# Optimization experiments

Measured on AMD Instinct MI355X. Metric: run time of the kernel, lower is better.

The kernel has to match this reference:

```python
import jax, jax.numpy as jnp
import numpy as np

B = 1048576
S = 8
K = 10  # n_facts
EPS = 1e-8
ENTROPY_W = 0.01
DIVERSITY_W = 0.1


def setup_inputs() -> dict:
    key = jax.random.key(0)
    k1, k2, k3, k4, k5 = jax.random.split(key, 5)
    p = jax.random.uniform(k1, (B, 2, K), dtype=jnp.float32) + 1e-3
    pCS = p / jnp.sum(p, axis=-1, keepdims=True)  # normalized probs like Categorical
    base_loss = jax.random.uniform(k2, (1,), dtype=jnp.float32)
    Y = jax.random.randint(k3, (B,), 0, 19, dtype=jnp.int32)
    samples1 = jax.random.randint(k4, (S, B), 0, K, dtype=jnp.int32)
    samples2 = jax.random.randint(k5, (S, B), 0, K, dtype=jnp.int32)
    return {"pCS": pCS, "base_loss": base_loss, "Y": Y,
            "samples1": samples1, "samples2": samples2}


def reference(pCS, base_loss, Y, samples1, samples2):
    n_facts = pCS.shape[-1]
    s = samples1.shape[0]
    p1 = pCS[:, 0, :]  # [B, K]
    p2 = pCS[:, 1, :]
    # entropy regularization
    ent1 = -jnp.sum(p1 * jnp.log(p1 + EPS), axis=-1).mean()
    ent2 = -jnp.sum(p2 * jnp.log(p2 + EPS), axis=-1).mean()
    entropy_loss = -(ent1 + ent2) / 2
    # diversity: count unique (d1,d2) pairs per batch element (vectorized bincount-style)
    pairs = (samples1 * n_facts + samples2).T  # [B, S]
    eq = pairs[:, :, None] == pairs[:, None, :]  # [B, S, S]
    earlier = jnp.tril(jnp.ones((s, s), dtype=bool), k=-1)  # j < i
    dup = jnp.any(eq & earlier[None], axis=-1)  # [B, S] True if seen before
    unique_counts = jnp.sum(~dup, axis=-1).astype(jnp.float32)  # [B]
    diversity = unique_counts.mean()
    max_diversity = min(s, n_facts * n_facts)
    diversity_ratio = diversity / max_diversity
    diversity_loss = -jnp.log(diversity_ratio + EPS)
    # REINFORCE leave-one-out (computed, not added to total in original)
    pred_labels = samples1 + samples2  # [S, B] (addition task)
    correct = (pred_labels == Y[None, :]).astype(jnp.float32)
    sample_acc = correct.mean()
    b_idx = jnp.arange(p1.shape[0])[None, :]
    log_probs = jnp.log(p1)[b_idx, samples1] + jnp.log(p2)[b_idx, samples2]  # [S, B]
    baseline = (jnp.sum(correct, axis=0, keepdims=True) - correct) / (s - 1 + EPS)
    advantage = jax.lax.stop_gradient(correct - baseline)
    rloo_loss = -jnp.mean(log_probs * advantage)
    total_loss = base_loss[0] + ENTROPY_W * entropy_loss + DIVERSITY_W * diversity_loss
    return jnp.stack([total_loss, rloo_loss, diversity_loss, sample_acc])
```

## Files before the change

### kernel.cpp

```cpp
#include <hip/hip_runtime.h>

#define S_CONST 8
#define EPSF 1e-8f

__device__ __forceinline__ void elem(int j, float p, const int a[S_CONST],
                                     float g[S_CONST], float& ent) {
    const float lg = __logf(p);
    ent += p * lg;
    #pragma unroll
    for (int s = 0; s < S_CONST; ++s) g[s] = (a[s] == j) ? lg : g[s];
}

__global__ __launch_bounds__(256) void fml_rows(
        const float* __restrict__ pCS,
        const int* __restrict__ Y,
        const int* __restrict__ s1g,
        const int* __restrict__ s2g,
        float4* __restrict__ partials,
        int B)
{
    float ent = 0.f, uniq = 0.f, corr = 0.f, rloo = 0.f;

    const int gid = blockIdx.x * 256 + threadIdx.x;
    const int gstride = gridDim.x * 256;

    #pragma unroll 1
    for (int row = gid; row < B; row += gstride) {
        const float4* rp = reinterpret_cast<const float4*>(pCS + (size_t)row * 20);
        const float4 v0 = rp[0], v1 = rp[1], v2 = rp[2], v3 = rp[3], v4 = rp[4];
        const int y = Y[row];
        int a1[S_CONST], a2[S_CONST];
        #pragma unroll
        for (int s = 0; s < S_CONST; ++s) {
            a1[s] = s1g[(size_t)s * B + row];
            a2[s] = s2g[(size_t)s * B + row];
        }

        float c[S_CONST], csum = 0.f;
        #pragma unroll
        for (int s = 0; s < S_CONST; ++s) {
            c[s] = (a1[s] + a2[s] == y) ? 1.f : 0.f;
            csum += c[s];
        }
        corr += csum;

        {
            int pr[S_CONST];
            #pragma unroll
            for (int s = 0; s < S_CONST; ++s) pr[s] = a1[s] * 10 + a2[s];
            #pragma unroll
            for (int i = 0; i < S_CONST; ++i) {
                bool dup = false;
                #pragma unroll
                for (int j = 0; j < i; ++j) dup = dup || (pr[i] == pr[j]);
                uniq += dup ? 0.f : 1.f;
            }
        }

        float adv[S_CONST];
        #pragma unroll
        for (int s = 0; s < S_CONST; ++s)
            adv[s] = c[s] * (8.0f / 7.0f) - csum * (1.0f / 7.0f);

        float g1[S_CONST];
        #pragma unroll
        for (int s = 0; s < S_CONST; ++s) g1[s] = 0.f;
        elem(0, v0.x, a1, g1, ent); elem(1, v0.y, a1, g1, ent);
        elem(2, v0.z, a1, g1, ent); elem(3, v0.w, a1, g1, ent);
        elem(4, v1.x, a1, g1, ent); elem(5, v1.y, a1, g1, ent);
        elem(6, v1.z, a1, g1, ent); elem(7, v1.w, a1, g1, ent);
        elem(8, v2.x, a1, g1, ent); elem(9, v2.y, a1, g1, ent);
        #pragma unroll
        for (int s = 0; s < S_CONST; ++s) rloo += g1[s] * adv[s];

        float g2[S_CONST];
        #pragma unroll
        for (int s = 0; s < S_CONST; ++s) g2[s] = 0.f;
        elem(0, v2.z, a2, g2, ent); elem(1, v2.w, a2, g2, ent);
        elem(2, v3.x, a2, g2, ent); elem(3, v3.y, a2, g2, ent);
        elem(4, v3.z, a2, g2, ent); elem(5, v3.w, a2, g2, ent);
        elem(6, v4.x, a2, g2, ent); elem(7, v4.y, a2, g2, ent);
        elem(8, v4.z, a2, g2, ent); elem(9, v4.w, a2, g2, ent);
        #pragma unroll
        for (int s = 0; s < S_CONST; ++s) rloo += g2[s] * adv[s];
    }

    #pragma unroll
    for (int off = 32; off >= 1; off >>= 1) {
        ent  += __shfl_xor(ent,  off);
        uniq += __shfl_xor(uniq, off);
        corr += __shfl_xor(corr, off);
        rloo += __shfl_xor(rloo, off);
    }

    __shared__ float red[4][4];
    const int lane = threadIdx.x & 63;
    const int wv   = threadIdx.x >> 6;
    if (lane == 0) {
        red[wv][0] = ent; red[wv][1] = uniq;
        red[wv][2] = corr; red[wv][3] = rloo;
    }
    __syncthreads();
    if (threadIdx.x == 0) {
        float4 p;
        p.x = red[0][0] + red[1][0] + red[2][0] + red[3][0];
        p.y = red[0][1] + red[1][1] + red[2][1] + red[3][1];
        p.z = red[0][2] + red[1][2] + red[2][2] + red[3][2];
        p.w = red[0][3] + red[1][3] + red[2][3] + red[3][3];
        partials[blockIdx.x] = p;
    }
}

__global__ __launch_bounds__(1024) void fml_finalize(
        const float4* __restrict__ partials,
        const float* __restrict__ base_loss,
        float* __restrict__ out, int B, int nblocks)
{
    __shared__ double red[16][4];
    double e = 0, u = 0, cs = 0, rl = 0;
    for (int i = threadIdx.x; i < nblocks; i += 1024) {
        const float4 p = partials[i];
        e += (double)p.x; u += (double)p.y; cs += (double)p.z; rl += (double)p.w;
    }
    #pragma unroll
    for (int off = 32; off >= 1; off >>= 1) {
        e  += __shfl_xor(e,  off);
        u  += __shfl_xor(u,  off);
        cs += __shfl_xor(cs, off);
        rl += __shfl_xor(rl, off);
    }
    const int lane = threadIdx.x & 63;
    const int wave = threadIdx.x >> 6;
    if (lane == 0) { red[wave][0] = e; red[wave][1] = u; red[wave][2] = cs; red[wave][3] = rl; }
    __syncthreads();
    if (threadIdx.x == 0) {
        e = 0; u = 0; cs = 0; rl = 0;
        #pragma unroll
        for (int w = 0; w < 16; ++w) {
            e += red[w][0]; u += red[w][1]; cs += red[w][2]; rl += red[w][3];
        }
        const double dB = (double)B;
        const float entropy_loss = (float)(e / (2.0 * dB));
        const float diversity = (float)(u / dB);
        const float ratio = diversity / 8.0f;
        const float diversity_loss = -logf(ratio + EPSF);
        const float sample_acc = (float)(cs / (dB * (double)S_CONST));
        const float rloo_loss  = (float)(-rl / (dB * (double)S_CONST));
        out[0] = base_loss[0] + 0.01f * entropy_loss + 0.1f * diversity_loss;
        out[1] = rloo_loss;
        out[2] = diversity_loss;
        out[3] = sample_acc;
    }
}

extern "C" void kernel_launch(void* const* d_in, const int* in_sizes, int n_in,
                              void* d_out, int out_size, void* d_ws, size_t ws_size,
                              hipStream_t stream) {
    const float* pCS       = (const float*)d_in[0];
    const float* base_loss = (const float*)d_in[1];
    const int*   Y         = (const int*)d_in[2];
    const int*   s1        = (const int*)d_in[3];
    const int*   s2        = (const int*)d_in[4];
    float* out = (float*)d_out;
    const int B = in_sizes[2];

    float4* partials = (float4*)d_ws;

    const int grid = 2048;
    fml_rows<<<grid, 256, 0, stream>>>(pCS, Y, s1, s2, partials, B);
    fml_finalize<<<1, 1024, 0, stream>>>(partials, base_loss, out, B, grid);
}
```

Measured before the change: 42.21 us.

## Double-buffer probability rows through LDS with async global-to-LDS loads

Replaces the grid-stride row loop with a per-wave pipeline. Each wave takes 4 chunks of 64 rows and stages their probability rows into double-buffered shared memory with global_load_lds DMA, using fully contiguous loads. The sample indices for the next chunk are prefetched into registers while the current chunk is computed. The aim is to hide memory latency and coalesce the strided 80-byte row reads. In exchange it relies on the compiler inserting correct waits for the LDS DMA, and it launches a fixed grid sized to the data instead of a persistent grid.

```diff
diff --git a/kernel.cpp b/kernel.cpp
--- a/kernel.cpp
+++ b/kernel.cpp
@@ -2,6 +2,47 @@
 
 #define S_CONST 8
 #define EPSF 1e-8f
+#define CPW 4
+#define WPB 4
+
+struct Samp { int y; int a1[S_CONST]; int a2[S_CONST]; };
+
+__device__ __forceinline__ void gload_lds16(const float* g, float* l) {
+    __builtin_amdgcn_global_load_lds(
+        (const __attribute__((address_space(1))) void*)g,
+        (__attribute__((address_space(3))) void*)l,
+        16, 0, 0);
+}
+
+__device__ __forceinline__ void stage(const float* __restrict__ pCS, float* buf,
+                                      int base, int B, int lane) {
+    const float* src = pCS + (size_t)base * 20;
+    const bool full = (base + 64) <= B;
+    #pragma unroll
+    for (int k = 0; k < 5; ++k) {
+        const int g = lane + (k << 6);
+        if (full || base + g / 5 < B)
+            gload_lds16(src + (size_t)g * 4, buf + (size_t)k * 256);
+    }
+}
+
+__device__ __forceinline__ void load_samp(Samp& sm, const int* __restrict__ Y,
+                                          const int* __restrict__ s1g,
+                                          const int* __restrict__ s2g,
+                                          int B, int row, bool inb) {
+    if (inb) {
+        sm.y = Y[row];
+        #pragma unroll
+        for (int s = 0; s < S_CONST; ++s) {
+            sm.a1[s] = s1g[(size_t)s * B + row];
+            sm.a2[s] = s2g[(size_t)s * B + row];
+        }
+    } else {
+        sm.y = -1;
+        #pragma unroll
+        for (int s = 0; s < S_CONST; ++s) { sm.a1[s] = 0; sm.a2[s] = 0; }
+    }
+}
 
 __device__ __forceinline__ void elem(int j, float p, const int a[S_CONST],
                                      float g[S_CONST], float& ent) {
@@ -11,78 +52,115 @@
     for (int s = 0; s < S_CONST; ++s) g[s] = (a[s] == j) ? lg : g[s];
 }
 
-__global__ __launch_bounds__(256) void fml_rows(
+__device__ __forceinline__ void compute(const float4& w0, const float4& w1,
+                                        const float4& w2, const float4& w3,
+                                        const float4& w4, const Samp& sm,
+                                        float& ent, float& uniq, float& corr,
+                                        float& rloo) {
+    float c[S_CONST], csum = 0.f;
+    #pragma unroll
+    for (int s = 0; s < S_CONST; ++s) {
+        c[s] = (sm.a1[s] + sm.a2[s] == sm.y) ? 1.f : 0.f;
+        csum += c[s];
+    }
+    corr += csum;
+
+    {
+        int pr[S_CONST];
+        #pragma unroll
+        for (int s = 0; s < S_CONST; ++s) pr[s] = sm.a1[s] * 10 + sm.a2[s];
+        #pragma unroll
+        for (int i = 0; i < S_CONST; ++i) {
+            bool dup = false;
+            #pragma unroll
+            for (int j = 0; j < i; ++j) dup = dup || (pr[i] == pr[j]);
+            uniq += dup ? 0.f : 1.f;
+        }
+    }
+
+    float adv[S_CONST];
+    #pragma unroll
+    for (int s = 0; s < S_CONST; ++s)
+        adv[s] = c[s] * (8.0f / 7.0f) - csum * (1.0f / 7.0f);
+
+    float g1[S_CONST];
+    #pragma unroll
+    for (int s = 0; s < S_CONST; ++s) g1[s] = 0.f;
+    elem(0, w0.x, sm.a1, g1, ent); elem(1, w0.y, sm.a1, g1, ent);
+    elem(2, w0.z, sm.a1, g1, ent); elem(3, w0.w, sm.a1, g1, ent);
+    elem(4, w1.x, sm.a1, g1, ent); elem(5, w1.y, sm.a1, g1, ent);
+    elem(6, w1.z, sm.a1, g1, ent); elem(7, w1.w, sm.a1, g1, ent);
+    elem(8, w2.x, sm.a1, g1, ent); elem(9, w2.y, sm.a1, g1, ent);
+    #pragma unroll
+    for (int s = 0; s < S_CONST; ++s) rloo += g1[s] * adv[s];
+
+    float g2[S_CONST];
+    #pragma unroll
+    for (int s = 0; s < S_CONST; ++s) g2[s] = 0.f;
+    elem(0, w2.z, sm.a2, g2, ent); elem(1, w2.w, sm.a2, g2, ent);
+    elem(2, w3.x, sm.a2, g2, ent); elem(3, w3.y, sm.a2, g2, ent);
+    elem(4, w3.z, sm.a2, g2, ent); elem(5, w3.w, sm.a2, g2, ent);
+    elem(6, w4.x, sm.a2, g2, ent); elem(7, w4.y, sm.a2, g2, ent);
+    elem(8, w4.z, sm.a2, g2, ent); elem(9, w4.w, sm.a2, g2, ent);
+    #pragma unroll
+    for (int s = 0; s < S_CONST; ++s) rloo += g2[s] * adv[s];
+}
+
+__global__ __launch_bounds__(256, 4) void fml_pipe(
         const float* __restrict__ pCS,
         const int* __restrict__ Y,
         const int* __restrict__ s1g,
         const int* __restrict__ s2g,
         float4* __restrict__ partials,
-        int B)
+        int B, int nchunks)
 {
+    __shared__ float pan[WPB][2][64 * 20];
+    __shared__ float red[WPB][4];
+
+    const int lane = threadIdx.x & 63;
+    const int wv   = threadIdx.x >> 6;
+    float* buf0 = pan[wv][0];
+    float* buf1 = pan[wv][1];
+
+    const int wid = blockIdx.x * WPB + wv;
+    const int c0  = wid * CPW;
+
     float ent = 0.f, uniq = 0.f, corr = 0.f, rloo = 0.f;
-
-    const int gid = blockIdx.x * 256 + threadIdx.x;
-    const int gstride = gridDim.x * 256;
-
-    #pragma unroll 1
-    for (int row = gid; row < B; row += gstride) {
-        const float4* rp = reinterpret_cast<const float4*>(pCS + (size_t)row * 20);
-        const float4 v0 = rp[0], v1 = rp[1], v2 = rp[2], v3 = rp[3], v4 = rp[4];
-        const int y = Y[row];
-        int a1[S_CONST], a2[S_CONST];
-        #pragma unroll
-        for (int s = 0; s < S_CONST; ++s) {
-            a1[s] = s1g[(size_t)s * B + row];
-            a2[s] = s2g[(size_t)s * B + row];
-        }
-
-        float c[S_CONST], csum = 0.f;
-        #pragma unroll
-        for (int s = 0; s < S_CONST; ++s) {
-            c[s] = (a1[s] + a2[s] == y) ? 1.f : 0.f;
-            csum += c[s];
-        }
-        corr += csum;
-
-        {
-            int pr[S_CONST];
-            #pragma unroll
-            for (int s = 0; s < S_CONST; ++s) pr[s] = a1[s] * 10 + a2[s];
-            #pragma unroll
-            for (int i = 0; i < S_CONST; ++i) {
-                bool dup = false;
-                #pragma unroll
-                for (int j = 0; j < i; ++j) dup = dup || (pr[i] == pr[j]);
-                uniq += dup ? 0.f : 1.f;
-            }
-        }
-
-        float adv[S_CONST];
-        #pragma unroll
-        for (int s = 0; s < S_CONST; ++s)
-            adv[s] = c[s] * (8.0f / 7.0f) - csum * (1.0f / 7.0f);
-
-        float g1[S_CONST];
-        #pragma unroll
-        for (int s = 0; s < S_CONST; ++s) g1[s] = 0.f;
-        elem(0, v0.x, a1, g1, ent); elem(1, v0.y, a1, g1, ent);
-        elem(2, v0.z, a1, g1, ent); elem(3, v0.w, a1, g1, ent);
-        elem(4, v1.x, a1, g1, ent); elem(5, v1.y, a1, g1, ent);
-        elem(6, v1.z, a1, g1, ent); elem(7, v1.w, a1, g1, ent);
-        elem(8, v2.x, a1, g1, ent); elem(9, v2.y, a1, g1, ent);
-        #pragma unroll
-        for (int s = 0; s < S_CONST; ++s) rloo += g1[s] * adv[s];
-
-        float g2[S_CONST];
-        #pragma unroll
-        for (int s = 0; s < S_CONST; ++s) g2[s] = 0.f;
-        elem(0, v2.z, a2, g2, ent); elem(1, v2.w, a2, g2, ent);
-        elem(2, v3.x, a2, g2, ent); elem(3, v3.y, a2, g2, ent);
-        elem(4, v3.z, a2, g2, ent); elem(5, v3.w, a2, g2, ent);
-        elem(6, v4.x, a2, g2, ent); elem(7, v4.y, a2, g2, ent);
-        elem(8, v4.z, a2, g2, ent); elem(9, v4.w, a2, g2, ent);
-        #pragma unroll
-        for (int s = 0; s < S_CONST; ++s) rloo += g2[s] * adv[s];
+    Samp sm[2];
+
+    if (c0 < nchunks)     stage(pCS, buf0, c0 << 6, B, lane);
+    if (c0 + 1 < nchunks) stage(pCS, buf1, (c0 + 1) << 6, B, lane);
+    {
+        const int base = c0 << 6;
+        const bool inb = (c0 < nchunks) && ((size_t)base + lane < (size_t)B);
+        load_samp(sm[0], Y, s1g, s2g, B, base + lane, inb);
+    }
+
+    #pragma unroll
+    for (int i = 0; i < CPW; ++i) {
+        const int cur = i & 1;
+        const int c = c0 + i;
+        const bool has = c < nchunks;
+        const int base = c << 6;
+        const bool inb = has && (base + lane < B);
+
+        float4 w0, w1, w2, w3, w4;
+        if (has) {
+            const float4* rp = reinterpret_cast<const float4*>(
+                (cur ? buf1 : buf0) + lane * 20);
+            w0 = rp[0]; w1 = rp[1]; w2 = rp[2]; w3 = rp[3]; w4 = rp[4];
+        }
+
+        if (i + 2 < CPW && c0 + i + 2 < nchunks)
+            stage(pCS, cur ? buf1 : buf0, (c0 + i + 2) << 6, B, lane);
+
+        if (i + 1 < CPW) {
+            const int bn = (c0 + i + 1) << 6;
+            const bool inbn = (c0 + i + 1 < nchunks) && (bn + lane < B);
+            load_samp(sm[(i + 1) & 1], Y, s1g, s2g, B, bn + lane, inbn);
+        }
+
+        if (inb) compute(w0, w1, w2, w3, w4, sm[cur], ent, uniq, corr, rloo);
     }
 
     #pragma unroll
@@ -93,9 +171,6 @@
         rloo += __shfl_xor(rloo, off);
     }
 
-    __shared__ float red[4][4];
-    const int lane = threadIdx.x & 63;
-    const int wv   = threadIdx.x >> 6;
     if (lane == 0) {
         red[wv][0] = ent; red[wv][1] = uniq;
         red[wv][2] = corr; red[wv][3] = rloo;
@@ -164,9 +239,12 @@
     float* out = (float*)d_out;
     const int B = in_sizes[2];
 
+    const int nchunks = (B + 63) >> 6;
+    const int waves   = (nchunks + CPW - 1) / CPW;
+    const int blocks  = (waves + WPB - 1) / WPB;
+
     float4* partials = (float4*)d_ws;
 
-    const int grid = 2048;
-    fml_rows<<<grid, 256, 0, stream>>>(pCS, Y, s1, s2, partials, B);
-    fml_finalize<<<1, 1024, 0, stream>>>(partials, base_loss, out, B, grid);
-}
+    fml_pipe<<<blocks, 256, 0, stream>>>(pCS, Y, s1, s2, partials, B, nchunks);
+    fml_finalize<<<1, 1024, 0, stream>>>(partials, base_loss, out, B, blocks);
+}
```

Result: no change. 42.80 us (+1.4%).
